# Performance work log

Measured on AMD Instinct MI355X. Metric: run time of the kernel, lower is better.

The kernel has to match this reference:

```python
import jax, jax.numpy as jnp
import numpy as np

N = 50000      # nodes
E = 250000     # edges (pairs) per key
DIN = 256
DOUT = 256
OH = 16        # one_hot_length
T = 2          # params['t']


def setup_inputs() -> dict:
    key = jax.random.key(0)
    ks = jax.random.split(key, 16)
    s_in = 1.0 / np.float32(np.sqrt(DIN))
    s_tr = 1.0 / np.float32(np.sqrt(DIN + OH))
    return {
        "h": jax.random.normal(ks[0], (N, DIN), jnp.float32),
        "pairs_k0": jax.random.randint(ks[1], (T, E), 0, N),
        "pairs_k1": jax.random.randint(ks[2], (T, E), 0, N),
        "degrees_k0": jax.random.uniform(ks[3], (T, E, OH), jnp.float32),
        "degrees_k1": jax.random.uniform(ks[4], (T, E, OH), jnp.float32),
        "scatter_k0": jax.random.randint(ks[5], (E,), 0, N),
        "scatter_k1": jax.random.randint(ks[6], (E,), 0, N),
        "W_lin": jax.random.normal(ks[7], (DIN, DOUT), jnp.float32) * s_in,
        "b_lin": jax.random.normal(ks[8], (DOUT,), jnp.float32) * 0.01,
        "W_k0": jax.random.normal(ks[9], (DIN + OH, DOUT), jnp.float32) * s_tr,
        "b_k0": jax.random.normal(ks[10], (DOUT,), jnp.float32) * 0.01,
        "W_k1": jax.random.normal(ks[11], (DIN + OH, DOUT), jnp.float32) * s_tr,
        "b_k1": jax.random.normal(ks[12], (DOUT,), jnp.float32) * 0.01,
        "eps_k0": jnp.zeros((1,), jnp.float32),
        "eps_k1": jnp.zeros((1,), jnp.float32),
    }


def _key_term(h, pairs, degrees, W, b, scatter, eps):
    # combination == 'multi': product over t of sigmoid(Linear([h[pairs_i], deg_i]))
    h_temp = jnp.ones((pairs.shape[1], W.shape[1]), h.dtype)
    for i in range(T):
        h_t = jnp.concatenate([h[pairs[i]], degrees[i]], axis=1)  # [E, DIN+OH]
        h_temp = h_temp * jax.nn.sigmoid(h_t @ W + b)             # [E, DOUT]
    h_sum = jax.ops.segment_sum(h_temp, scatter, num_segments=N)  # [N, DOUT]
    return (1.0 + eps) * h_sum                                    # scalar eps (shape [1])


def reference(h, pairs_k0, pairs_k1, degrees_k0, degrees_k1,
              scatter_k0, scatter_k1, W_lin, b_lin,
              W_k0, b_k0, W_k1, b_k1, eps_k0, eps_k1):
    h3 = h @ W_lin + b_lin
    h3 = h3 + _key_term(h, pairs_k0, degrees_k0, W_k0, b_k0, scatter_k0, eps_k0)
    h3 = h3 + _key_term(h, pairs_k1, degrees_k1, W_k1, b_k1, scatter_k1, eps_k1)
    return h3
```

## Files before the change

### kernel.cpp

```cpp
#include <hip/hip_runtime.h>
#include <hip/hip_bf16.h>

#define N_NODES 50000
#define N_EDGES 250000
#define DIN_ 256
#define DOUT_ 256
#define OH_ 16
#define KF_ 288
#define NBLK_EDGE ((N_EDGES + 63) / 64)
#define NBLK_G ((N_NODES + 63) / 64)
#define SCAN_TOT (2 * N_NODES)
#define SCAN_NB ((SCAN_TOT + 255) / 256)
#define NB_CONV ((N_NODES * DIN_ / 8) / 256)
#define NB_PREP ((DOUT_ * KF_ + 255) / 256)
#define NB_HIST ((N_EDGES + 255) / 256)

typedef short short8 __attribute__((ext_vector_type(8)));
typedef float f32x4 __attribute__((ext_vector_type(4)));

__device__ __forceinline__ unsigned short f2bf(float f) {
    unsigned u = __builtin_bit_cast(unsigned, f);
    return (unsigned short)((u + 0x7fffu + ((u >> 16) & 1u)) >> 16);
}

__device__ __forceinline__ float bf2f(unsigned v) {
    return __builtin_bit_cast(float, v << 16);
}

__device__ __forceinline__ uint4 pack8(float f0, float f1, float f2, float f3,
                                       float f4, float f5, float f6, float f7) {
    uint4 u;
    u.x = (unsigned)f2bf(f0) | ((unsigned)f2bf(f1) << 16);
    u.y = (unsigned)f2bf(f2) | ((unsigned)f2bf(f3) << 16);
    u.z = (unsigned)f2bf(f4) | ((unsigned)f2bf(f5) << 16);
    u.w = (unsigned)f2bf(f6) | ((unsigned)f2bf(f7) << 16);
    return u;
}

__device__ __forceinline__ float fast_rcp(float x) {
#if __has_builtin(__builtin_amdgcn_rcpf)
    return __builtin_amdgcn_rcpf(x);
#else
    return 1.0f / x;
#endif
}

__device__ __forceinline__ void gl_lds16(const void* g, void* l) {
    __builtin_amdgcn_global_load_lds(
        (const __attribute__((address_space(1))) unsigned int*)g,
        (__attribute__((address_space(3))) unsigned int*)l, 16, 0, 0);
}

__global__ void fused_prep(const float* __restrict__ h, unsigned short* __restrict__ hbf,
                           const float* __restrict__ W_lin,
                           const float* __restrict__ W_k0,
                           const float* __restrict__ W_k1,
                           unsigned short* __restrict__ WT_lin,
                           unsigned short* __restrict__ WT_k0,
                           unsigned short* __restrict__ WT_k1,
                           const int* __restrict__ sc0, const int* __restrict__ sc1,
                           int* __restrict__ hist) {
    int bx = blockIdx.x;
    if (bx < NB_CONV) {
        int idx = bx * 256 + threadIdx.x;
        const f32x4* s = (const f32x4*)(h + (size_t)idx * 8);
        f32x4 a = s[0], b = s[1];
        ((uint4*)hbf)[idx] = pack8(a[0], a[1], a[2], a[3], b[0], b[1], b[2], b[3]);
    } else if (bx < NB_CONV + NB_PREP) {
        int idx = (bx - NB_CONV) * 256 + threadIdx.x;
        if (idx < DOUT_ * DIN_) {
            int n = idx >> 8, k = idx & 255;
            WT_lin[idx] = f2bf(W_lin[k * DOUT_ + n]);
        }
        if (idx < DOUT_ * KF_) {
            int n = idx / KF_, k = idx - n * KF_;
            float v0 = 0.f, v1 = 0.f;
            if (k < DIN_ + OH_) {
                v0 = W_k0[k * DOUT_ + n];
                v1 = W_k1[k * DOUT_ + n];
            }
            WT_k0[idx] = f2bf(v0);
            WT_k1[idx] = f2bf(v1);
        }
    } else {
        int e = (bx - NB_CONV - NB_PREP) * 256 + threadIdx.x;
        if (e < N_EDGES) {
            atomicAdd(&hist[sc0[e]], 1);
            atomicAdd(&hist[N_NODES + sc1[e]], 1);
        }
    }
}

__global__ void scan_pass1(const int* __restrict__ hist, int* __restrict__ partials) {
    __shared__ int sdata[256];
    int gid = blockIdx.x * 256 + threadIdx.x;
    sdata[threadIdx.x] = (gid < SCAN_TOT) ? hist[gid] : 0;
    __syncthreads();
    for (int d = 128; d > 0; d >>= 1) {
        if (threadIdx.x < d) sdata[threadIdx.x] += sdata[threadIdx.x + d];
        __syncthreads();
    }
    if (threadIdx.x == 0) partials[blockIdx.x] = sdata[0];
}

__global__ __launch_bounds__(512) void scan_pass2(int* __restrict__ partials) {
    __shared__ int s[512];
    int t = threadIdx.x;
    s[t] = (t < SCAN_NB) ? partials[t] : 0;
    __syncthreads();
    for (int d = 1; d < 512; d <<= 1) {
        int add = (t >= d) ? s[t - d] : 0;
        __syncthreads();
        s[t] += add;
        __syncthreads();
    }
    if (t < SCAN_NB) partials[t] = (t == 0) ? 0 : s[t - 1];
}

__global__ void scan_pass3(const int* __restrict__ hist, const int* __restrict__ partials,
                           int* __restrict__ offs) {
    __shared__ int s[256];
    int gid = blockIdx.x * 256 + threadIdx.x;
    int t = threadIdx.x;
    int v = (gid < SCAN_TOT) ? hist[gid] : 0;
    s[t] = v;
    __syncthreads();
    for (int d = 1; d < 256; d <<= 1) {
        int add = (t >= d) ? s[t - d] : 0;
        __syncthreads();
        s[t] += add;
        __syncthreads();
    }
    if (gid < SCAN_TOT) offs[gid] = partials[blockIdx.x] + s[t] - v;
}

__global__ __launch_bounds__(256) void rank_lin(const int* __restrict__ sc0,
                                                const int* __restrict__ sc1,
                                                int* __restrict__ offs,
                                                int* __restrict__ order,
                                                int* __restrict__ keys,
                                                const unsigned short* __restrict__ hbf,
                                                const unsigned short* __restrict__ WT_lin,
                                                const unsigned short* __restrict__ WTk0,
                                                const unsigned short* __restrict__ WTk1,
                                                const float* __restrict__ b_lin,
                                                const float* __restrict__ bk0,
                                                const float* __restrict__ bk1,
                                                float* __restrict__ out,
                                                unsigned short* __restrict__ G0,
                                                unsigned short* __restrict__ G1) {
    if (blockIdx.x >= 3 * NBLK_G) {
        int e = (blockIdx.x - 3 * NBLK_G) * 256 + threadIdx.x;
        if (e < N_EDGES) {
            int k0 = sc0[e];
            int p = atomicAdd(&offs[k0], 1);
            order[p] = e; keys[p] = k0;
            int k1 = sc1[e];
            int q = atomicAdd(&offs[N_NODES + k1], 1);
            order[q] = e; keys[q] = k1;
        }
        return;
    }
    __shared__ unsigned short Alds[2][64][32];
    __shared__ unsigned short Blds[2][256][32];
    __shared__ float bias_lds[256];
    int kb = blockIdx.x / NBLK_G;
    int bx = blockIdx.x - kb * NBLK_G;
    const unsigned short* WT; const float* bias; int stride;
    if (kb == 0)      { WT = WTk0;   bias = bk0;   stride = KF_; }
    else if (kb == 1) { WT = WTk1;   bias = bk1;   stride = KF_; }
    else              { WT = WT_lin; bias = b_lin; stride = DIN_; }

    int tid = threadIdx.x;
    int w = tid >> 6, ln = tid & 63, l15 = ln & 15;
    int row0 = bx * 64;
    bias_lds[tid] = bias[tid];

    int ar = row0 + w * 16 + (ln >> 2);
    if (ar >= N_NODES) ar = N_NODES - 1;
    int qs = (ln & 3) ^ ((ln >> 3) & 3);
    const unsigned short* asrc = hbf + (size_t)ar * DIN_ + qs * 8;
    int brow = w * 64;
    int swz = ((ln >> 4) ^ ((l15 >> 1) & 3)) * 8;

    f32x4 acc[16];
#pragma unroll
    for (int j = 0; j < 16; ++j) acc[j] = (f32x4)(0.f);

    gl_lds16(asrc, &Alds[0][w * 16][0]);
#pragma unroll
    for (int i = 0; i < 4; ++i) {
        int n = brow + i * 16 + (ln >> 2);
        gl_lds16(WT + (size_t)n * stride + qs * 8, &Blds[0][brow + i * 16][0]);
    }
    __syncthreads();

    int buf = 0;
    for (int kk = 0; kk < 8; ++kk) {
        if (kk < 7) {
            gl_lds16(asrc + (kk + 1) * 32, &Alds[buf ^ 1][w * 16][0]);
#pragma unroll
            for (int i = 0; i < 4; ++i) {
                int n = brow + i * 16 + (ln >> 2);
                gl_lds16(WT + (size_t)n * stride + (kk + 1) * 32 + qs * 8,
                         &Blds[buf ^ 1][brow + i * 16][0]);
            }
        }
        short8 af = *(const short8*)&Alds[buf][w * 16 + l15][swz];
#pragma unroll
        for (int j = 0; j < 16; ++j) {
            short8 bf = *(const short8*)&Blds[buf][j * 16 + l15][swz];
            acc[j] = __builtin_amdgcn_mfma_f32_16x16x32_bf16(af, bf, acc[j], 0, 0, 0);
        }
        __syncthreads();
        buf ^= 1;
    }

    int rbase = row0 + w * 16 + ((ln >> 4) << 2);
    unsigned short* G = (kb == 0) ? G0 : G1;
#pragma unroll
    for (int j = 0; j < 16; ++j) {
        int n = j * 16 + l15;
        float bv = bias_lds[n];
#pragma unroll
        for (int i = 0; i < 4; ++i) {
            int rr = rbase + i;
            if (rr < N_NODES) {
                float v = acc[j][i] + bv;
                if (kb == 2) out[(size_t)rr * DOUT_ + n] = v;
                else         G[(size_t)rr * DOUT_ + n] = f2bf(v);
            }
        }
    }
}

__global__ __launch_bounds__(256, 4) void edge_fused(const unsigned short* __restrict__ Gk0,
                                                     const unsigned short* __restrict__ Gk1,
                                                     const int* __restrict__ pairs0,
                                                     const int* __restrict__ pairs1,
                                                     const float* __restrict__ deg0,
                                                     const float* __restrict__ deg1,
                                                     const int* __restrict__ order_all,
                                                     const int* __restrict__ keys_all,
                                                     const unsigned short* __restrict__ WT0,
                                                     const unsigned short* __restrict__ WT1,
                                                     const float* __restrict__ eps0,
                                                     const float* __restrict__ eps1,
                                                     float* __restrict__ out) {
    __shared__ unsigned int Dlds[4][16][132];
    __shared__ float FL[4][64][2];
    __shared__ int tgt[64], pl0[64], pl1[64], el[64];
    int kb = (blockIdx.x >= NBLK_EDGE) ? 1 : 0;
    int bx = blockIdx.x - kb * NBLK_EDGE;
    const unsigned short* G = kb ? Gk1 : Gk0;
    const int* pairs = kb ? pairs1 : pairs0;
    const float* degrees = kb ? deg1 : deg0;
    const int* order_k = order_all + kb * N_EDGES;
    const int* keys_k  = keys_all + kb * N_EDGES;
    const unsigned short* WT = kb ? WT1 : WT0;
    float epv = 1.0f + (kb ? eps1[0] : eps0[0]);

    int tid = threadIdx.x;
    int w = tid >> 6, ln = tid & 63, l15 = ln & 15, ks = ln >> 4;
    int e0 = bx * 64;
    if (tid < 64) {
        int s = e0 + tid;
        int sc = (s < N_EDGES) ? s : N_EDGES - 1;
        int e = __builtin_nontemporal_load(order_k + sc);
        el[tid]  = e;
        tgt[tid] = (s < N_EDGES) ? __builtin_nontemporal_load(keys_k + s) : -1;
        pl0[tid] = __builtin_nontemporal_load(pairs + e);
        pl1[tid] = __builtin_nontemporal_load(pairs + N_EDGES + e);
    }
    __syncthreads();

    int eA = el[w * 16 + l15];
    f32x4 xa = (f32x4)(0.f), xb = xa, ya = xa, yb = xa;
    if (ks < 2) {
        const f32x4* s0 = (const f32x4*)(degrees + (size_t)eA * OH_ + ks * 8);
        const f32x4* s1 = (const f32x4*)(degrees + ((size_t)N_EDGES + eA) * OH_ + ks * 8);
        xa = __builtin_nontemporal_load(s0);
        xb = __builtin_nontemporal_load(s0 + 1);
        ya = __builtin_nontemporal_load(s1);
        yb = __builtin_nontemporal_load(s1 + 1);
    }

    unsigned int gv[4][16];
#pragma unroll
    for (int r = 0; r < 16; ++r) {
        int row = w * 16 + r;
        const unsigned int* b0 = (const unsigned int*)(G + (size_t)pl0[row] * DOUT_) + ln;
        const unsigned int* b1 = (const unsigned int*)(G + (size_t)pl1[row] * DOUT_) + ln;
        gv[0][r] = b0[0];
        gv[1][r] = b1[0];
        gv[2][r] = b0[64];
        gv[3][r] = b1[64];
    }
    asm volatile("" ::: "memory");

    short8 a0f = __builtin_bit_cast(short8, pack8(xa[0], xa[1], xa[2], xa[3],
                                                  xb[0], xb[1], xb[2], xb[3]));
    short8 a1f = __builtin_bit_cast(short8, pack8(ya[0], ya[1], ya[2], ya[3],
                                                  yb[0], yb[1], yb[2], yb[3]));
    if (ks >= 2) { a0f = (short8)0; a1f = (short8)0; }

#define MFMA_PHASE(p)                                                                  \
    {                                                                                  \
        f32x4 acc0[8], acc1[8];                                                        \
        _Pragma("unroll")                                                              \
        for (int j = 0; j < 8; ++j) { acc0[j] = (f32x4)(0.f); acc1[j] = (f32x4)(0.f); }\
        _Pragma("unroll")                                                              \
        for (int j = 0; j < 8; ++j) {                                                  \
            int n = (p) * 128 + j * 16 + l15;                                          \
            short8 bf = (short8)0;                                                     \
            if (ks < 2) bf = *(const short8*)(WT + (size_t)n * KF_ + 256 + ks * 8);    \
            acc0[j] = __builtin_amdgcn_mfma_f32_16x16x32_bf16(a0f, bf, acc0[j], 0,0,0);\
            acc1[j] = __builtin_amdgcn_mfma_f32_16x16x32_bf16(a1f, bf, acc1[j], 0,0,0);\
        }                                                                              \
        _Pragma("unroll")                                                              \
        for (int j = 0; j < 8; ++j) {                                                  \
            _Pragma("unroll")                                                          \
            for (int i = 0; i < 4; ++i) {                                              \
                Dlds[w][ks * 4 + i][j * 16 + l15] = (unsigned)f2bf(acc0[j][i])         \
                                                  | ((unsigned)f2bf(acc1[j][i]) << 16);\
            }                                                                          \
        }                                                                              \
    }

#define FLUSH(p, key, r0, r1)                                                          \
    if ((key) >= 0) {                                                                  \
        FL[w][ln][0] = (r0);                                                           \
        FL[w][ln][1] = (r1);                                                           \
        float va = FL[w][(ln >> 1)][ln & 1];                                           \
        float vb = FL[w][32 + (ln >> 1)][ln & 1];                                      \
        atomicAdd(&out[(size_t)(key) * DOUT_ + (p) * 128 + ln], va);                   \
        atomicAdd(&out[(size_t)(key) * DOUT_ + (p) * 128 + 64 + ln], vb);              \
    }

#define REDUCE_PHASE(p, gva, gvb)                                                      \
    {                                                                                  \
        int runkey = tgt[w * 16];                                                      \
        float rs0 = 0.f, rs1 = 0.f;                                                    \
        _Pragma("unroll")                                                              \
        for (int r = 0; r < 16; ++r) {                                                 \
            int row = w * 16 + r;                                                      \
            uint2 dp = *(const uint2*)&Dlds[w][r][2 * ln];                             \
            unsigned int g0u = (gva)[r], g1u = (gvb)[r];                               \
            float la0 = bf2f(g0u & 0xffffu) + bf2f(dp.x & 0xffffu);                    \
            float la1 = bf2f(g1u & 0xffffu) + bf2f(dp.x >> 16);                        \
            float ha0 = bf2f(g0u >> 16) + bf2f(dp.y & 0xffffu);                        \
            float ha1 = bf2f(g1u >> 16) + bf2f(dp.y >> 16);                            \
            float v0 = epv * fast_rcp((1.f + __expf(-la0)) * (1.f + __expf(-la1)));    \
            float v1 = epv * fast_rcp((1.f + __expf(-ha0)) * (1.f + __expf(-ha1)));    \
            int k = tgt[row];                                                          \
            if (k != runkey) {                                                         \
                FLUSH(p, runkey, rs0, rs1);                                            \
                runkey = k; rs0 = v0; rs1 = v1;                                        \
            } else { rs0 += v0; rs1 += v1; }                                           \
        }                                                                              \
        FLUSH(p, runkey, rs0, rs1);                                                    \
    }

    MFMA_PHASE(0);
    REDUCE_PHASE(0, gv[0], gv[1]);
    MFMA_PHASE(1);
    REDUCE_PHASE(1, gv[2], gv[3]);

#undef MFMA_PHASE
#undef FLUSH
#undef REDUCE_PHASE
}

extern "C" void kernel_launch(void* const* d_in, const int* in_sizes, int n_in,
                              void* d_out, int out_size, void* d_ws, size_t ws_size,
                              hipStream_t stream) {
    const float* h        = (const float*)d_in[0];
    const int*   pairs_k0 = (const int*)d_in[1];
    const int*   pairs_k1 = (const int*)d_in[2];
    const float* deg_k0   = (const float*)d_in[3];
    const float* deg_k1   = (const float*)d_in[4];
    const int*   sc_k0    = (const int*)d_in[5];
    const int*   sc_k1    = (const int*)d_in[6];
    const float* W_lin    = (const float*)d_in[7];
    const float* b_lin    = (const float*)d_in[8];
    const float* W_k0     = (const float*)d_in[9];
    const float* b_k0     = (const float*)d_in[10];
    const float* W_k1     = (const float*)d_in[11];
    const float* b_k1     = (const float*)d_in[12];
    const float* eps_k0   = (const float*)d_in[13];
    const float* eps_k1   = (const float*)d_in[14];
    float* out = (float*)d_out;

    size_t ush_elems = (size_t)DOUT_ * DIN_ + 2 * (size_t)DOUT_ * KF_
                     + 3 * (size_t)N_NODES * DIN_;
    size_t int_elems = 2 * (size_t)N_NODES * 2 + 2 * (size_t)N_EDGES * 2 + 512;
    size_t need = ush_elems * sizeof(unsigned short) + int_elems * sizeof(int);
    if (ws_size < need) return;

    unsigned short* WT_lin = (unsigned short*)d_ws;
    unsigned short* WT_k0  = WT_lin + DOUT_ * DIN_;
    unsigned short* WT_k1  = WT_k0 + DOUT_ * KF_;
    unsigned short* h_bf   = WT_k1 + DOUT_ * KF_;
    unsigned short* G0     = h_bf + (size_t)N_NODES * DIN_;
    unsigned short* G1     = G0 + (size_t)N_NODES * DIN_;
    int* hist     = (int*)(G1 + (size_t)N_NODES * DIN_);
    int* offs     = hist + 2 * N_NODES;
    int* order    = offs + 2 * N_NODES;
    int* keys     = order + 2 * N_EDGES;
    int* partials = keys + 2 * N_EDGES;

    hipMemsetAsync(hist, 0, 2 * N_NODES * sizeof(int), stream);
    fused_prep<<<NB_CONV + NB_PREP + NB_HIST, 256, 0, stream>>>(
        h, h_bf, W_lin, W_k0, W_k1, WT_lin, WT_k0, WT_k1, sc_k0, sc_k1, hist);
    scan_pass1<<<SCAN_NB, 256, 0, stream>>>(hist, partials);
    scan_pass2<<<1, 512, 0, stream>>>(partials);
    scan_pass3<<<SCAN_NB, 256, 0, stream>>>(hist, partials, offs);
    rank_lin<<<3 * NBLK_G + NB_HIST, 256, 0, stream>>>(
        sc_k0, sc_k1, offs, order, keys, h_bf, WT_lin, WT_k0, WT_k1,
        b_lin, b_k0, b_k1, out, G0, G1);
    edge_fused<<<2 * NBLK_EDGE, 256, 0, stream>>>(G0, G1, pairs_k0, pairs_k1,
                                                  deg_k0, deg_k1, order, keys,
                                                  WT_k0, WT_k1, eps_k0, eps_k1, out);
}
```

Measured before the change: 369.4 us.

## Restructure edge kernel to per-node-block ownership with LDS accumulation

Replaces the edge-parallel fused kernel, which scattered results into the output with global atomics, with a node-parallel kernel. Each block owns 16 destination nodes, walks their sorted edge ranges for both keys in chunks of 32, accumulates in shared memory with LDS atomics, and does a single read-modify-write of the output. This removes global atomic traffic at the cost of smaller MFMA tiles, more barriers per chunk, and load imbalance from varying per-node degree. The partially filled tail chunk of each block also wastes work.

New measurement: 464.8 us. 25.8% more time.

```diff
diff --git a/kernel.cpp b/kernel.cpp
--- a/kernel.cpp
+++ b/kernel.cpp
@@ -7,13 +7,14 @@
 #define DOUT_ 256
 #define OH_ 16
 #define KF_ 288
-#define NBLK_EDGE ((N_EDGES + 63) / 64)
 #define NBLK_G ((N_NODES + 63) / 64)
 #define SCAN_TOT (2 * N_NODES)
 #define SCAN_NB ((SCAN_TOT + 255) / 256)
 #define NB_CONV ((N_NODES * DIN_ / 8) / 256)
 #define NB_PREP ((DOUT_ * KF_ + 255) / 256)
 #define NB_HIST ((N_EDGES + 255) / 256)
+#define NODE_BLK 16
+#define NBLK_NODE (N_NODES / NODE_BLK)
 
 typedef short short8 __attribute__((ext_vector_type(8)));
 typedef float f32x4 __attribute__((ext_vector_type(4)));
@@ -234,141 +235,145 @@
     }
 }
 
-__global__ __launch_bounds__(256, 4) void edge_fused(const unsigned short* __restrict__ Gk0,
-                                                     const unsigned short* __restrict__ Gk1,
-                                                     const int* __restrict__ pairs0,
-                                                     const int* __restrict__ pairs1,
-                                                     const float* __restrict__ deg0,
-                                                     const float* __restrict__ deg1,
-                                                     const int* __restrict__ order_all,
-                                                     const int* __restrict__ keys_all,
-                                                     const unsigned short* __restrict__ WT0,
-                                                     const unsigned short* __restrict__ WT1,
-                                                     const float* __restrict__ eps0,
-                                                     const float* __restrict__ eps1,
-                                                     float* __restrict__ out) {
-    __shared__ unsigned int Dlds[4][16][132];
-    __shared__ float FL[4][64][2];
-    __shared__ int tgt[64], pl0[64], pl1[64], el[64];
-    int kb = (blockIdx.x >= NBLK_EDGE) ? 1 : 0;
-    int bx = blockIdx.x - kb * NBLK_EDGE;
-    const unsigned short* G = kb ? Gk1 : Gk0;
-    const int* pairs = kb ? pairs1 : pairs0;
-    const float* degrees = kb ? deg1 : deg0;
-    const int* order_k = order_all + kb * N_EDGES;
-    const int* keys_k  = keys_all + kb * N_EDGES;
-    const unsigned short* WT = kb ? WT1 : WT0;
-    float epv = 1.0f + (kb ? eps1[0] : eps0[0]);
-
-    int tid = threadIdx.x;
-    int w = tid >> 6, ln = tid & 63, l15 = ln & 15, ks = ln >> 4;
-    int e0 = bx * 64;
-    if (tid < 64) {
-        int s = e0 + tid;
-        int sc = (s < N_EDGES) ? s : N_EDGES - 1;
-        int e = __builtin_nontemporal_load(order_k + sc);
-        el[tid]  = e;
-        tgt[tid] = (s < N_EDGES) ? __builtin_nontemporal_load(keys_k + s) : -1;
-        pl0[tid] = __builtin_nontemporal_load(pairs + e);
-        pl1[tid] = __builtin_nontemporal_load(pairs + N_EDGES + e);
+__global__ __launch_bounds__(256, 4) void edge_node(const unsigned short* __restrict__ Gk0,
+                                                    const unsigned short* __restrict__ Gk1,
+                                                    const int* __restrict__ pairs0,
+                                                    const int* __restrict__ pairs1,
+                                                    const float* __restrict__ deg0,
+                                                    const float* __restrict__ deg1,
+                                                    const int* __restrict__ order_g,
+                                                    const int* __restrict__ keys_g,
+                                                    const int* __restrict__ offs_v,
+                                                    const unsigned short* __restrict__ WT0,
+                                                    const unsigned short* __restrict__ WT1,
+                                                    const float* __restrict__ eps0,
+                                                    const float* __restrict__ eps1,
+                                                    float* __restrict__ out) {
+    __shared__ float accL[NODE_BLK][260];
+    __shared__ unsigned int Dlds[32][132];
+    __shared__ int el_c[32], tg_c[32], p0_c[32], p1_c[32];
+
+    int n0 = blockIdx.x * NODE_BLK;
+    int tid = threadIdx.x, w = tid >> 6, ln = tid & 63, l15 = ln & 15, ks = ln >> 4;
+
+    for (int i = tid; i < NODE_BLK * 260; i += 256) (&accL[0][0])[i] = 0.f;
+
+    for (int kb = 0; kb < 2; ++kb) {
+        const unsigned short* G = kb ? Gk1 : Gk0;
+        const int* pairs = kb ? pairs1 : pairs0;
+        const float* degrees = kb ? deg1 : deg0;
+        const unsigned short* WT = kb ? WT1 : WT0;
+        float epv = 1.0f + (kb ? eps1[0] : eps0[0]);
+        int i0 = kb * N_NODES + n0;
+        int gs = (i0 == 0) ? 0 : offs_v[i0 - 1];
+        int ge = offs_v[i0 + NODE_BLK - 1];
+
+        for (int cs = gs; cs < ge; cs += 32) {
+            __syncthreads();
+            if (tid < 32) {
+                int s = cs + tid;
+                int e;
+                if (s < ge) {
+                    e = __builtin_nontemporal_load(order_g + s);
+                    tg_c[tid] = __builtin_nontemporal_load(keys_g + s) - n0;
+                } else {
+                    e = __builtin_nontemporal_load(order_g + (ge - 1));
+                    tg_c[tid] = -1;
+                }
+                el_c[tid] = e;
+                p0_c[tid] = pairs[e];
+                p1_c[tid] = pairs[N_EDGES + e];
+            }
+            __syncthreads();
+
+            unsigned int gv[4][8];
+#pragma unroll
+            for (int r = 0; r < 8; ++r) {
+                int slot = w * 8 + r;
+                const unsigned int* b0 = (const unsigned int*)(G + (size_t)p0_c[slot] * DOUT_) + ln;
+                const unsigned int* b1 = (const unsigned int*)(G + (size_t)p1_c[slot] * DOUT_) + ln;
+                gv[0][r] = b0[0];
+                gv[1][r] = b1[0];
+                gv[2][r] = b0[64];
+                gv[3][r] = b1[64];
+            }
+            asm volatile("" ::: "memory");
+
+            short8 afr[2][2];
+#pragma unroll
+            for (int rt = 0; rt < 2; ++rt) {
+                f32x4 xa = (f32x4)(0.f), xb = xa, ya = xa, yb = xa;
+                int eA = el_c[rt * 16 + l15];
+                if (ks < 2) {
+                    const f32x4* s0 = (const f32x4*)(degrees + (size_t)eA * OH_ + ks * 8);
+                    const f32x4* s1 = (const f32x4*)(degrees + ((size_t)N_EDGES + eA) * OH_ + ks * 8);
+                    xa = __builtin_nontemporal_load(s0);
+                    xb = __builtin_nontemporal_load(s0 + 1);
+                    ya = __builtin_nontemporal_load(s1);
+                    yb = __builtin_nontemporal_load(s1 + 1);
+                }
+                afr[rt][0] = __builtin_bit_cast(short8, pack8(xa[0], xa[1], xa[2], xa[3],
+                                                              xb[0], xb[1], xb[2], xb[3]));
+                afr[rt][1] = __builtin_bit_cast(short8, pack8(ya[0], ya[1], ya[2], ya[3],
+                                                              yb[0], yb[1], yb[2], yb[3]));
+                if (ks >= 2) { afr[rt][0] = (short8)0; afr[rt][1] = (short8)0; }
+            }
+
+#pragma unroll
+            for (int p = 0; p < 2; ++p) {
+#pragma unroll
+                for (int jj = 0; jj < 2; ++jj) {
+                    int n = p * 128 + (w * 2 + jj) * 16 + l15;
+                    short8 bf = (short8)0;
+                    if (ks < 2) bf = *(const short8*)(WT + (size_t)n * KF_ + 256 + ks * 8);
+#pragma unroll
+                    for (int rt = 0; rt < 2; ++rt) {
+                        f32x4 a0 = (f32x4)(0.f), a1 = (f32x4)(0.f);
+                        a0 = __builtin_amdgcn_mfma_f32_16x16x32_bf16(afr[rt][0], bf, a0, 0, 0, 0);
+                        a1 = __builtin_amdgcn_mfma_f32_16x16x32_bf16(afr[rt][1], bf, a1, 0, 0, 0);
+#pragma unroll
+                        for (int i = 0; i < 4; ++i)
+                            Dlds[rt * 16 + ks * 4 + i][(w * 2 + jj) * 16 + l15] =
+                                (unsigned)f2bf(a0[i]) | ((unsigned)f2bf(a1[i]) << 16);
+                    }
+                }
+                __syncthreads();
+
+                int runkey = -1; float rs0 = 0.f, rs1 = 0.f;
+#pragma unroll
+                for (int r = 0; r < 8; ++r) {
+                    int slot = w * 8 + r;
+                    uint2 dp = *(const uint2*)&Dlds[slot][2 * ln];
+                    unsigned g0u = gv[2 * p][r], g1u = gv[2 * p + 1][r];
+                    float la0 = bf2f(g0u & 0xffffu) + bf2f(dp.x & 0xffffu);
+                    float la1 = bf2f(g1u & 0xffffu) + bf2f(dp.x >> 16);
+                    float ha0 = bf2f(g0u >> 16) + bf2f(dp.y & 0xffffu);
+                    float ha1 = bf2f(g1u >> 16) + bf2f(dp.y >> 16);
+                    float v0 = fast_rcp((1.f + __expf(-la0)) * (1.f + __expf(-la1)));
+                    float v1 = fast_rcp((1.f + __expf(-ha0)) * (1.f + __expf(-ha1)));
+                    int k = tg_c[slot];
+                    if (k != runkey) {
+                        if (runkey >= 0) {
+                            atomicAdd(&accL[runkey][p * 128 + 2 * ln], epv * rs0);
+                            atomicAdd(&accL[runkey][p * 128 + 2 * ln + 1], epv * rs1);
+                        }
+                        runkey = k; rs0 = v0; rs1 = v1;
+                    } else { rs0 += v0; rs1 += v1; }
+                }
+                if (runkey >= 0) {
+                    atomicAdd(&accL[runkey][p * 128 + 2 * ln], epv * rs0);
+                    atomicAdd(&accL[runkey][p * 128 + 2 * ln + 1], epv * rs1);
+                }
+                __syncthreads();
+            }
+        }
     }
     __syncthreads();
-
-    int eA = el[w * 16 + l15];
-    f32x4 xa = (f32x4)(0.f), xb = xa, ya = xa, yb = xa;
-    if (ks < 2) {
-        const f32x4* s0 = (const f32x4*)(degrees + (size_t)eA * OH_ + ks * 8);
-        const f32x4* s1 = (const f32x4*)(degrees + ((size_t)N_EDGES + eA) * OH_ + ks * 8);
-        xa = __builtin_nontemporal_load(s0);
-        xb = __builtin_nontemporal_load(s0 + 1);
-        ya = __builtin_nontemporal_load(s1);
-        yb = __builtin_nontemporal_load(s1 + 1);
-    }
-
-    unsigned int gv[4][16];
-#pragma unroll
-    for (int r = 0; r < 16; ++r) {
-        int row = w * 16 + r;
-        const unsigned int* b0 = (const unsigned int*)(G + (size_t)pl0[row] * DOUT_) + ln;
-        const unsigned int* b1 = (const unsigned int*)(G + (size_t)pl1[row] * DOUT_) + ln;
-        gv[0][r] = b0[0];
-        gv[1][r] = b1[0];
-        gv[2][r] = b0[64];
-        gv[3][r] = b1[64];
-    }
-    asm volatile("" ::: "memory");
-
-    short8 a0f = __builtin_bit_cast(short8, pack8(xa[0], xa[1], xa[2], xa[3],
-                                                  xb[0], xb[1], xb[2], xb[3]));
-    short8 a1f = __builtin_bit_cast(short8, pack8(ya[0], ya[1], ya[2], ya[3],
-                                                  yb[0], yb[1], yb[2], yb[3]));
-    if (ks >= 2) { a0f = (short8)0; a1f = (short8)0; }
-
-#define MFMA_PHASE(p)                                                                  \
-    {                                                                                  \
-        f32x4 acc0[8], acc1[8];                                                        \
-        _Pragma("unroll")                                                              \
-        for (int j = 0; j < 8; ++j) { acc0[j] = (f32x4)(0.f); acc1[j] = (f32x4)(0.f); }\
-        _Pragma("unroll")                                                              \
-        for (int j = 0; j < 8; ++j) {                                                  \
-            int n = (p) * 128 + j * 16 + l15;                                          \
-            short8 bf = (short8)0;                                                     \
-            if (ks < 2) bf = *(const short8*)(WT + (size_t)n * KF_ + 256 + ks * 8);    \
-            acc0[j] = __builtin_amdgcn_mfma_f32_16x16x32_bf16(a0f, bf, acc0[j], 0,0,0);\
-            acc1[j] = __builtin_amdgcn_mfma_f32_16x16x32_bf16(a1f, bf, acc1[j], 0,0,0);\
-        }                                                                              \
-        _Pragma("unroll")                                                              \
-        for (int j = 0; j < 8; ++j) {                                                  \
-            _Pragma("unroll")                                                          \
-            for (int i = 0; i < 4; ++i) {                                              \
-                Dlds[w][ks * 4 + i][j * 16 + l15] = (unsigned)f2bf(acc0[j][i])         \
-                                                  | ((unsigned)f2bf(acc1[j][i]) << 16);\
-            }                                                                          \
-        }                                                                              \
-    }
-
-#define FLUSH(p, key, r0, r1)                                                          \
-    if ((key) >= 0) {                                                                  \
-        FL[w][ln][0] = (r0);                                                           \
-        FL[w][ln][1] = (r1);                                                           \
-        float va = FL[w][(ln >> 1)][ln & 1];                                           \
-        float vb = FL[w][32 + (ln >> 1)][ln & 1];                                      \
-        atomicAdd(&out[(size_t)(key) * DOUT_ + (p) * 128 + ln], va);                   \
-        atomicAdd(&out[(size_t)(key) * DOUT_ + (p) * 128 + 64 + ln], vb);              \
-    }
-
-#define REDUCE_PHASE(p, gva, gvb)                                                      \
-    {                                                                                  \
-        int runkey = tgt[w * 16];                                                      \
-        float rs0 = 0.f, rs1 = 0.f;                                                    \
-        _Pragma("unroll")                                                              \
-        for (int r = 0; r < 16; ++r) {                                                 \
-            int row = w * 16 + r;                                                      \
-            uint2 dp = *(const uint2*)&Dlds[w][r][2 * ln];                             \
-            unsigned int g0u = (gva)[r], g1u = (gvb)[r];                               \
-            float la0 = bf2f(g0u & 0xffffu) + bf2f(dp.x & 0xffffu);                    \
-            float la1 = bf2f(g1u & 0xffffu) + bf2f(dp.x >> 16);                        \
-            float ha0 = bf2f(g0u >> 16) + bf2f(dp.y & 0xffffu);                        \
-            float ha1 = bf2f(g1u >> 16) + bf2f(dp.y >> 16);                            \
-            float v0 = epv * fast_rcp((1.f + __expf(-la0)) * (1.f + __expf(-la1)));    \
-            float v1 = epv * fast_rcp((1.f + __expf(-ha0)) * (1.f + __expf(-ha1)));    \
-            int k = tgt[row];                                                          \
-            if (k != runkey) {                                                         \
-                FLUSH(p, runkey, rs0, rs1);                                            \
-                runkey = k; rs0 = v0; rs1 = v1;                                        \
-            } else { rs0 += v0; rs1 += v1; }                                           \
-        }                                                                              \
-        FLUSH(p, runkey, rs0, rs1);                                                    \
-    }
-
-    MFMA_PHASE(0);
-    REDUCE_PHASE(0, gv[0], gv[1]);
-    MFMA_PHASE(1);
-    REDUCE_PHASE(1, gv[2], gv[3]);
-
-#undef MFMA_PHASE
-#undef FLUSH
-#undef REDUCE_PHASE
+#pragma unroll
+    for (int i = 0; i < NODE_BLK; ++i) {
+        size_t idx = (size_t)(n0 + i) * DOUT_ + tid;
+        out[idx] = out[idx] + accL[i][tid];
+    }
 }
 
 extern "C" void kernel_launch(void* const* d_in, const int* in_sizes, int n_in,
@@ -418,7 +423,7 @@
     rank_lin<<<3 * NBLK_G + NB_HIST, 256, 0, stream>>>(
         sc_k0, sc_k1, offs, order, keys, h_bf, WT_lin, WT_k0, WT_k1,
         b_lin, b_k0, b_k1, out, G0, G1);
-    edge_fused<<<2 * NBLK_EDGE, 256, 0, stream>>>(G0, G1, pairs_k0, pairs_k1,
-                                                  deg_k0, deg_k1, order, keys,
-                                                  WT_k0, WT_k1, eps_k0, eps_k1, out);
-}
+    edge_node<<<NBLK_NODE, 256, 0, stream>>>(G0, G1, pairs_k0, pairs_k1,
+                                             deg_k0, deg_k1, order, keys, offs,
+                                             WT_k0, WT_k1, eps_k0, eps_k1, out);
+}
```
